# Kernel optimization log

Hardware: AMD Instinct MI355X
Metric: run time of the kernel (lower is better)

The kernel has to match this reference:

```python
import jax, jax.numpy as jnp
import numpy as np

C0 = 32   # number of 0e (scalar) channels
C1 = 16   # number of 1o (vector) channels
NG = 1024 # num_graphs
N = 300000
F = C0 * (C0 + 1) // 2 + C1 * (C1 + 1) // 2  # 664 invariant outputs of TensorSquare->0e


def setup_inputs() -> dict:
    key = jax.random.key(0)
    k1, k2, k3 = jax.random.split(key, 3)
    node_ft = jax.random.normal(k1, (N, C0 + 3 * C1), dtype=jnp.float32)
    batch_index = jnp.sort(jax.random.randint(k2, (N,), 0, NG, dtype=jnp.int32))
    # o3.Linear-style init: normal / sqrt(fan_in)
    W = jax.random.normal(k3, (F, 1), dtype=jnp.float32) / np.float32(np.sqrt(F))
    return {"node_ft": node_ft, "batch_index": batch_index, "num_graphs": NG, "W": W}


def tensor_square_0e(node_ft):
    # Equivariant tensor square keeping only 0e (invariant) outputs:
    #  - symmetric products of scalar channels s_i * s_j (i<=j)
    #  - dot products of vector channels v_i . v_j (i<=j), component-normalized
    s = node_ft[:, :C0]                      # [N, C0]
    v = node_ft[:, C0:].reshape(-1, C1, 3)   # [N, C1, 3]
    i0, j0 = jnp.triu_indices(C0)
    i1, j1 = jnp.triu_indices(C1)
    ts_s = s[:, i0] * s[:, j0]                                  # [N, 528]
    vdot = jnp.einsum('nic,njc->nij', v, v) / jnp.float32(np.sqrt(3.0))
    ts_v = vdot[:, i1, j1]                                      # [N, 136]
    return jnp.concatenate([ts_s, ts_v], axis=1)                # [N, 664]


def reference(node_ft, batch_index, num_graphs, W):
    x = tensor_square_0e(node_ft)            # [N, F]
    x = jax.nn.selu(x)
    x = x @ W                                # [N, 1] attention logits (1x0e)
    ex = jnp.exp(x)                          # [N, 1]
    z = jax.ops.segment_sum(ex, batch_index, num_segments=num_graphs)  # [G, 1]
    attn = ex / z[batch_index]               # segment softmax weights [N, 1]
    out = jax.ops.segment_sum(node_ft * attn, batch_index, num_segments=num_graphs)
    return out                               # [G, C0 + 3*C1]
```

## Files before the change

kernel.cpp:

```cpp
#include <hip/hip_runtime.h>


typedef float f2 __attribute__((ext_vector_type(2)));

#define C0 32
#define C1 16
#define NODE_F 80
#define NG_CONST 1024

#define SELU_SCALE 1.0507009873554804934193349852946
#define SELU_ALPHA 1.6732632423543772848170429916717
#define LOG2E      1.4426950408889634073599246810019

#define CS_SCALE 1.2011224087864498f
#define CV_SCALE 0.91271231102878545f

#define KS(i, j) ((i) * C0 - ((i) * ((i) -1)) / 2 + ((j) - (i)))
#define KV(i, j) (528 + (i) * C1 - ((i) * ((i) -1)) / 2 + ((j) - (i)))

__global__ __launch_bounds__(256, 4) void pass1_logits(
    const float* __restrict__ nf, const float* __restrict__ W,
    float* __restrict__ ex_out, int N)
{
    __shared__ float4 buf[128 * 20];
    const int tid = threadIdx.x;
    const int base_row = blockIdx.x * 256;
    const int total4 = N * 20;
    const float4* g4 = (const float4*)nf;

    float4 row4[20];
    const int half = tid >> 7;
    const int r    = tid & 127;

    #pragma unroll
    for (int it = 0; it < 10; ++it) {
        int g = base_row * 20 + it * 256 + tid;
        buf[it * 256 + tid] = g4[g < total4 ? g : 0];
    }
    __syncthreads();
    if (half == 0) {
        const float4* src = &buf[r * 20];
        #pragma unroll
        for (int q = 0; q < 20; ++q) row4[q] = src[q];
    }
    __syncthreads();
    #pragma unroll
    for (int it = 0; it < 10; ++it) {
        int g = (base_row + 128) * 20 + it * 256 + tid;
        buf[it * 256 + tid] = g4[g < total4 ? g : 0];
    }
    __syncthreads();
    if (half == 1) {
        const float4* src = &buf[r * 20];
        #pragma unroll
        for (int q = 0; q < 20; ++q) row4[q] = src[q];
    }

    const float* row = (const float*)row4;

    f2 accA[2], accB[2];
    accA[0] = 0.f; accA[1] = 0.f; accB[0] = 0.f; accB[1] = 0.f;

    {
        f2 s2[C0 / 2];
        #pragma unroll
        for (int q = 0; q < C0 / 2; ++q)
            s2[q] = f2{row[2 * q], row[2 * q + 1]} * CS_SCALE;

        #pragma unroll
        for (int i = 0; i < C0; ++i) {
            const float si = (i & 1) ? s2[i >> 1].y : s2[i >> 1].x;
            const f2 si2 = f2{si, si};
            #pragma unroll
            for (int q = i / 2; q < C0 / 2; ++q) {
                f2 f = si2 * s2[q];
                f2 p = __builtin_elementwise_max(f, (f2)0.f);
                f2 m = __builtin_elementwise_min(f, (f2)0.f);
                f2 e; e.x = __builtin_amdgcn_exp2f(m.x);
                      e.y = __builtin_amdgcn_exp2f(m.y);
                f2 w;
                w.x = (2 * q >= i) ? W[KS(i, 2 * q)] : 0.0f;
                w.y = W[KS(i, 2 * q + 1)];
                accA[q & 1] = __builtin_elementwise_fma(w, p, accA[q & 1]);
                accB[q & 1] = __builtin_elementwise_fma(w, e, accB[q & 1]);
            }
        }
    }

    {
        f2 vp[C1 / 2][3];
        #pragma unroll
        for (int q = 0; q < C1 / 2; ++q) {
            #pragma unroll
            for (int c = 0; c < 3; ++c)
                vp[q][c] = f2{row[C0 + 6 * q + c], row[C0 + 6 * q + 3 + c]} * CV_SCALE;
        }
        #pragma unroll
        for (int i = 0; i < C1; ++i) {
            const int iq = i >> 1;
            float vi0 = (i & 1) ? vp[iq][0].y : vp[iq][0].x;
            float vi1 = (i & 1) ? vp[iq][1].y : vp[iq][1].x;
            float vi2 = (i & 1) ? vp[iq][2].y : vp[iq][2].x;
            #pragma unroll
            for (int q = i / 2; q < C1 / 2; ++q) {
                f2 f = f2{vi0, vi0} * vp[q][0];
                f = __builtin_elementwise_fma(f2{vi1, vi1}, vp[q][1], f);
                f = __builtin_elementwise_fma(f2{vi2, vi2}, vp[q][2], f);
                f2 p = __builtin_elementwise_max(f, (f2)0.f);
                f2 m = __builtin_elementwise_min(f, (f2)0.f);
                f2 e; e.x = __builtin_amdgcn_exp2f(m.x);
                      e.y = __builtin_amdgcn_exp2f(m.y);
                f2 w;
                w.x = (2 * q >= i) ? W[KV(i, 2 * q)] : 0.0f;
                w.y = W[KV(i, 2 * q + 1)];
                accA[q & 1] = __builtin_elementwise_fma(w, p, accA[q & 1]);
                accB[q & 1] = __builtin_elementwise_fma(w, e, accB[q & 1]);
            }
        }
    }

    const float A1 = accA[0].x + accA[0].y + accA[1].x + accA[1].y;
    const float A2 = accB[0].x + accB[0].y + accB[1].x + accB[1].y;
    const float l2 = fmaf((float)SELU_SCALE, A1,
                          (float)(SELU_SCALE * SELU_ALPHA * LOG2E) * A2);
    const int n = base_row + tid;
    if (n < N) ex_out[n] = __builtin_amdgcn_exp2f(l2);
}

__global__ __launch_bounds__(256) void seg_bounds_kernel(
    const int* __restrict__ bi, int* __restrict__ bounds, int N)
{
    const int g = blockIdx.x * blockDim.x + threadIdx.x;
    if (g > NG_CONST) return;
    int lo = 0, hi = N;
    while (lo < hi) {
        int mid = (lo + hi) >> 1;
        if (bi[mid] < g) lo = mid + 1; else hi = mid;
    }
    bounds[g] = lo;
}

#define P2T 640

__global__ __launch_bounds__(P2T) void pass2_pool(
    const float* __restrict__ nf, const float* __restrict__ ex,
    const int* __restrict__ bounds, float* __restrict__ out)
{
    __shared__ float4 red4[P2T];
    __shared__ float  zred[P2T];
    const int g = blockIdx.x;
    const int tid = threadIdx.x;
    const int start = bounds[g];
    const int end   = bounds[g + 1];

    const int no = tid / 20;
    const int c4 = tid % 20;
    const float4* nf4 = (const float4*)nf;

    float4 a0 = make_float4(0.f, 0.f, 0.f, 0.f), a1 = a0;
    float  z0 = 0.f, z1 = 0.f;
    int n = start + no;
    for (; n + 32 < end; n += 64) {
        float  w0 = ex[n];
        float4 v0 = nf4[(size_t)n * 20 + c4];
        float  w1 = ex[n + 32];
        float4 v1 = nf4[(size_t)(n + 32) * 20 + c4];
        a0.x = fmaf(v0.x, w0, a0.x); a0.y = fmaf(v0.y, w0, a0.y);
        a0.z = fmaf(v0.z, w0, a0.z); a0.w = fmaf(v0.w, w0, a0.w);
        z0 += w0;
        a1.x = fmaf(v1.x, w1, a1.x); a1.y = fmaf(v1.y, w1, a1.y);
        a1.z = fmaf(v1.z, w1, a1.z); a1.w = fmaf(v1.w, w1, a1.w);
        z1 += w1;
    }
    if (n < end) {
        float  w0 = ex[n];
        float4 v0 = nf4[(size_t)n * 20 + c4];
        a0.x = fmaf(v0.x, w0, a0.x); a0.y = fmaf(v0.y, w0, a0.y);
        a0.z = fmaf(v0.z, w0, a0.z); a0.w = fmaf(v0.w, w0, a0.w);
        z0 += w0;
    }
    a0.x += a1.x; a0.y += a1.y; a0.z += a1.z; a0.w += a1.w;
    z0 += z1;

    red4[tid] = a0;
    zred[tid] = z0;
    __syncthreads();
    #pragma unroll
    for (int s = 16; s > 0; s >>= 1) {
        if (no < s) {
            float4 o = red4[tid + s * 20];
            red4[tid].x += o.x; red4[tid].y += o.y;
            red4[tid].z += o.z; red4[tid].w += o.w;
            zred[tid] += zred[tid + s * 20];
        }
        __syncthreads();
    }
    if (tid < 20) {
        float z = zred[tid];
        float inv_z = (z > 0.0f) ? (1.0f / z) : 0.0f;
        float4 r = red4[tid];
        r.x *= inv_z; r.y *= inv_z; r.z *= inv_z; r.w *= inv_z;
        ((float4*)(out + (size_t)g * NODE_F))[tid] = r;
    }
}

extern "C" void kernel_launch(void* const* d_in, const int* in_sizes, int n_in,
                              void* d_out, int out_size, void* d_ws, size_t ws_size,
                              hipStream_t stream) {
    const float* nf = (const float*)d_in[0];
    const int*   bi = (const int*)d_in[1];
    const float* W  = (const float*)d_in[3];
    float* out = (float*)d_out;

    const int N = in_sizes[0] / NODE_F;
    float* ex     = (float*)d_ws;
    int*   bounds = (int*)d_ws + N;

    hipLaunchKernelGGL(seg_bounds_kernel, dim3((NG_CONST + 256) / 256), dim3(256),
                       0, stream, bi, bounds, N);
    hipLaunchKernelGGL(pass1_logits, dim3((N + 255) / 256), dim3(256),
                       0, stream, nf, W, ex, N);
    hipLaunchKernelGGL(pass2_pool, dim3(NG_CONST), dim3(P2T),
                       0, stream, nf, ex, bounds, out);
}
```

Baseline: 201.9 us.

## Stage node features column-major in LDS and use rolled loops with padded W table

```diff
diff --git a/kernel.cpp b/kernel.cpp
--- a/kernel.cpp
+++ b/kernel.cpp
@@ -15,129 +15,132 @@
 #define CS_SCALE 1.2011224087864498f
 #define CV_SCALE 0.91271231102878545f
 
-#define KS(i, j) ((i) * C0 - ((i) * ((i) -1)) / 2 + ((j) - (i)))
-#define KV(i, j) (528 + (i) * C1 - ((i) * ((i) -1)) / 2 + ((j) - (i)))
-
-__global__ __launch_bounds__(256, 4) void pass1_logits(
-    const float* __restrict__ nf, const float* __restrict__ W,
+__device__ __forceinline__ int ks_idx(int i, int j) { return i * C0 - (i * (i - 1)) / 2 + (j - i); }
+__device__ __forceinline__ int kv_idx(int i, int j) { return 528 + i * C1 - (i * (i - 1)) / 2 + (j - i); }
+
+#define WS_OFF_WS 0
+#define WS_OFF_WV 1024
+#define WS_OFF_EX 1280
+
+__global__ __launch_bounds__(256) void prep_kernel(
+    const int* __restrict__ bi, const float* __restrict__ W,
+    float* __restrict__ ws, int* __restrict__ bounds, int N)
+{
+    const int t = blockIdx.x * blockDim.x + threadIdx.x;
+    if (t <= NG_CONST) {
+        int lo = 0, hi = N;
+        while (lo < hi) {
+            int mid = (lo + hi) >> 1;
+            if (bi[mid] < t) lo = mid + 1; else hi = mid;
+        }
+        bounds[t] = lo;
+    } else if (t < 1025 + 512) {
+        int u = t - 1025;
+        int i = u >> 4, q = u & 15;
+        int j0 = 2 * q, j1 = 2 * q + 1;
+        float x = (j0 >= i) ? W[ks_idx(i, j0)] : 0.0f;
+        float y = (j1 >= i) ? W[ks_idx(i, j1)] : 0.0f;
+        ws[WS_OFF_WS + 2 * u]     = x;
+        ws[WS_OFF_WS + 2 * u + 1] = y;
+    } else if (t < 1025 + 512 + 128) {
+        int u = t - 1537;
+        int i = u >> 3, q = u & 7;
+        int j0 = 2 * q, j1 = 2 * q + 1;
+        float x = (j0 >= i) ? W[kv_idx(i, j0)] : 0.0f;
+        float y = (j1 >= i) ? W[kv_idx(i, j1)] : 0.0f;
+        ws[WS_OFF_WV + 2 * u]     = x;
+        ws[WS_OFF_WV + 2 * u + 1] = y;
+    }
+}
+
+__global__ __launch_bounds__(256, 3) void pass1_logits(
+    const float* __restrict__ nf, const float* __restrict__ ws,
     float* __restrict__ ex_out, int N)
 {
-    __shared__ float4 buf[128 * 20];
-    const int tid = threadIdx.x;
-    const int base_row = blockIdx.x * 256;
-    const int total4 = N * 20;
+    __shared__ float lds[48 * 256];
+    const int tid  = threadIdx.x;
+    const int base = blockIdx.x * 256;
     const float4* g4 = (const float4*)nf;
-
-    float4 row4[20];
-    const int half = tid >> 7;
-    const int r    = tid & 127;
+    const f2* Ws = (const f2*)(ws + WS_OFF_WS);
+    const f2* Wv = (const f2*)(ws + WS_OFF_WV);
 
     #pragma unroll
-    for (int it = 0; it < 10; ++it) {
-        int g = base_row * 20 + it * 256 + tid;
-        buf[it * 256 + tid] = g4[g < total4 ? g : 0];
-    }
-    __syncthreads();
-    if (half == 0) {
-        const float4* src = &buf[r * 20];
-        #pragma unroll
-        for (int q = 0; q < 20; ++q) row4[q] = src[q];
-    }
-    __syncthreads();
+    for (int it = 0; it < 8; ++it) {
+        int idx = it * 256 + tid;
+        int r = idx >> 3, c4 = idx & 7;
+        int row = base + r; if (row > N - 1) row = N - 1;
+        float4 v = g4[(size_t)row * 20 + c4];
+        lds[(4 * c4 + 0) * 256 + r] = v.x * CS_SCALE;
+        lds[(4 * c4 + 1) * 256 + r] = v.y * CS_SCALE;
+        lds[(4 * c4 + 2) * 256 + r] = v.z * CS_SCALE;
+        lds[(4 * c4 + 3) * 256 + r] = v.w * CS_SCALE;
+    }
+    __syncthreads();
+
+    f2 accA = (f2)0.f, accB = (f2)0.f;
+
+    #pragma clang loop unroll(disable)
+    for (int i = 0; i < C0; ++i) {
+        const float si = lds[i * 256 + tid];
+        const f2* wrow = Ws + i * 16;
+        #pragma unroll 2
+        for (int q = i >> 1; q < 16; ++q) {
+            f2 sj = f2{lds[(2 * q) * 256 + tid], lds[(2 * q + 1) * 256 + tid]};
+            f2 f = sj * f2{si, si};
+            f2 p = __builtin_elementwise_max(f, (f2)0.f);
+            f2 m = __builtin_elementwise_min(f, (f2)0.f);
+            f2 e; e.x = __builtin_amdgcn_exp2f(m.x);
+                  e.y = __builtin_amdgcn_exp2f(m.y);
+            f2 w = wrow[q];
+            accA = __builtin_elementwise_fma(w, p, accA);
+            accB = __builtin_elementwise_fma(w, e, accB);
+        }
+    }
+    __syncthreads();
+
     #pragma unroll
-    for (int it = 0; it < 10; ++it) {
-        int g = (base_row + 128) * 20 + it * 256 + tid;
-        buf[it * 256 + tid] = g4[g < total4 ? g : 0];
-    }
-    __syncthreads();
-    if (half == 1) {
-        const float4* src = &buf[r * 20];
-        #pragma unroll
-        for (int q = 0; q < 20; ++q) row4[q] = src[q];
-    }
-
-    const float* row = (const float*)row4;
-
-    f2 accA[2], accB[2];
-    accA[0] = 0.f; accA[1] = 0.f; accB[0] = 0.f; accB[1] = 0.f;
-
-    {
-        f2 s2[C0 / 2];
-        #pragma unroll
-        for (int q = 0; q < C0 / 2; ++q)
-            s2[q] = f2{row[2 * q], row[2 * q + 1]} * CS_SCALE;
-
-        #pragma unroll
-        for (int i = 0; i < C0; ++i) {
-            const float si = (i & 1) ? s2[i >> 1].y : s2[i >> 1].x;
-            const f2 si2 = f2{si, si};
-            #pragma unroll
-            for (int q = i / 2; q < C0 / 2; ++q) {
-                f2 f = si2 * s2[q];
-                f2 p = __builtin_elementwise_max(f, (f2)0.f);
-                f2 m = __builtin_elementwise_min(f, (f2)0.f);
-                f2 e; e.x = __builtin_amdgcn_exp2f(m.x);
-                      e.y = __builtin_amdgcn_exp2f(m.y);
-                f2 w;
-                w.x = (2 * q >= i) ? W[KS(i, 2 * q)] : 0.0f;
-                w.y = W[KS(i, 2 * q + 1)];
-                accA[q & 1] = __builtin_elementwise_fma(w, p, accA[q & 1]);
-                accB[q & 1] = __builtin_elementwise_fma(w, e, accB[q & 1]);
-            }
-        }
-    }
-
-    {
-        f2 vp[C1 / 2][3];
-        #pragma unroll
-        for (int q = 0; q < C1 / 2; ++q) {
-            #pragma unroll
-            for (int c = 0; c < 3; ++c)
-                vp[q][c] = f2{row[C0 + 6 * q + c], row[C0 + 6 * q + 3 + c]} * CV_SCALE;
-        }
-        #pragma unroll
-        for (int i = 0; i < C1; ++i) {
-            const int iq = i >> 1;
-            float vi0 = (i & 1) ? vp[iq][0].y : vp[iq][0].x;
-            float vi1 = (i & 1) ? vp[iq][1].y : vp[iq][1].x;
-            float vi2 = (i & 1) ? vp[iq][2].y : vp[iq][2].x;
-            #pragma unroll
-            for (int q = i / 2; q < C1 / 2; ++q) {
-                f2 f = f2{vi0, vi0} * vp[q][0];
-                f = __builtin_elementwise_fma(f2{vi1, vi1}, vp[q][1], f);
-                f = __builtin_elementwise_fma(f2{vi2, vi2}, vp[q][2], f);
-                f2 p = __builtin_elementwise_max(f, (f2)0.f);
-                f2 m = __builtin_elementwise_min(f, (f2)0.f);
-                f2 e; e.x = __builtin_amdgcn_exp2f(m.x);
-                      e.y = __builtin_amdgcn_exp2f(m.y);
-                f2 w;
-                w.x = (2 * q >= i) ? W[KV(i, 2 * q)] : 0.0f;
-                w.y = W[KV(i, 2 * q + 1)];
-                accA[q & 1] = __builtin_elementwise_fma(w, p, accA[q & 1]);
-                accB[q & 1] = __builtin_elementwise_fma(w, e, accB[q & 1]);
-            }
-        }
-    }
-
-    const float A1 = accA[0].x + accA[0].y + accA[1].x + accA[1].y;
-    const float A2 = accB[0].x + accB[0].y + accB[1].x + accB[1].y;
+    for (int it = 0; it < 12; ++it) {
+        int idx = it * 256 + tid;
+        int r = idx / 12, c4 = idx % 12;
+        int row = base + r; if (row > N - 1) row = N - 1;
+        float4 v = g4[(size_t)row * 20 + 8 + c4];
+        lds[(4 * c4 + 0) * 256 + r] = v.x * CV_SCALE;
+        lds[(4 * c4 + 1) * 256 + r] = v.y * CV_SCALE;
+        lds[(4 * c4 + 2) * 256 + r] = v.z * CV_SCALE;
+        lds[(4 * c4 + 3) * 256 + r] = v.w * CV_SCALE;
+    }
+    __syncthreads();
+
+    #pragma clang loop unroll(disable)
+    for (int i = 0; i < C1; ++i) {
+        const float vi0 = lds[(3 * i + 0) * 256 + tid];
+        const float vi1 = lds[(3 * i + 1) * 256 + tid];
+        const float vi2 = lds[(3 * i + 2) * 256 + tid];
+        const f2* wrow = Wv + i * 8;
+        #pragma unroll 2
+        for (int q = i >> 1; q < 8; ++q) {
+            f2 vj0 = f2{lds[(6 * q + 0) * 256 + tid], lds[(6 * q + 3) * 256 + tid]};
+            f2 vj1 = f2{lds[(6 * q + 1) * 256 + tid], lds[(6 * q + 4) * 256 + tid]};
+            f2 vj2 = f2{lds[(6 * q + 2) * 256 + tid], lds[(6 * q + 5) * 256 + tid]};
+            f2 f = vj0 * f2{vi0, vi0};
+            f = __builtin_elementwise_fma(vj1, f2{vi1, vi1}, f);
+            f = __builtin_elementwise_fma(vj2, f2{vi2, vi2}, f);
+            f2 p = __builtin_elementwise_max(f, (f2)0.f);
+            f2 m = __builtin_elementwise_min(f, (f2)0.f);
+            f2 e; e.x = __builtin_amdgcn_exp2f(m.x);
+                  e.y = __builtin_amdgcn_exp2f(m.y);
+            f2 w = wrow[q];
+            accA = __builtin_elementwise_fma(w, p, accA);
+            accB = __builtin_elementwise_fma(w, e, accB);
+        }
+    }
+
+    const float A1 = accA.x + accA.y;
+    const float A2 = accB.x + accB.y;
     const float l2 = fmaf((float)SELU_SCALE, A1,
                           (float)(SELU_SCALE * SELU_ALPHA * LOG2E) * A2);
-    const int n = base_row + tid;
+    const int n = base + tid;
     if (n < N) ex_out[n] = __builtin_amdgcn_exp2f(l2);
-}
-
-__global__ __launch_bounds__(256) void seg_bounds_kernel(
-    const int* __restrict__ bi, int* __restrict__ bounds, int N)
-{
-    const int g = blockIdx.x * blockDim.x + threadIdx.x;
-    if (g > NG_CONST) return;
-    int lo = 0, hi = N;
-    while (lo < hi) {
-        int mid = (lo + hi) >> 1;
-        if (bi[mid] < g) lo = mid + 1; else hi = mid;
-    }
-    bounds[g] = lo;
 }
 
 #define P2T 640
@@ -213,13 +216,13 @@
     float* out = (float*)d_out;
 
     const int N = in_sizes[0] / NODE_F;
-    float* ex     = (float*)d_ws;
-    int*   bounds = (int*)d_ws + N;
-
-    hipLaunchKernelGGL(seg_bounds_kernel, dim3((NG_CONST + 256) / 256), dim3(256),
-                       0, stream, bi, bounds, N);
-    hipLaunchKernelGGL(pass1_logits, dim3((N + 255) / 256), dim3(256),
-                       0, stream, nf, W, ex, N);
-    hipLaunchKernelGGL(pass2_pool, dim3(NG_CONST), dim3(P2T),
-                       0, stream, nf, ex, bounds, out);
-}
+    float* ws     = (float*)d_ws;
+    float* ex     = ws + WS_OFF_EX;
+    int*   bounds = (int*)(ws + WS_OFF_EX + N);
+
+    hipLaunchKernelGGL(prep_kernel, dim3(7), dim3(256), 0, stream, bi, W, ws, bounds, N);
+    hipLaunchKernelGGL(pass1_logits, dim3((N + 255) / 256), dim3(256), 0, stream,
+                       nf, ws, ex, N);
+    hipLaunchKernelGGL(pass2_pool, dim3(NG_CONST), dim3(P2T), 0, stream,
+                       nf, ex, bounds, out);
+}
```

After: 221.0 us. 9.4% more time.

## Fuse logits and pooling into one kernel with atomic segment accumulation

Applied to the files above, without the earlier changes.

```diff
diff --git a/kernel.cpp b/kernel.cpp
--- a/kernel.cpp
+++ b/kernel.cpp
@@ -7,6 +7,7 @@
 #define C1 16
 #define NODE_F 80
 #define NG_CONST 1024
+#define NPB 320
 
 #define SELU_SCALE 1.0507009873554804934193349852946
 #define SELU_ALPHA 1.6732632423543772848170429916717
@@ -15,78 +16,91 @@
 #define CS_SCALE 1.2011224087864498f
 #define CV_SCALE 0.91271231102878545f
 
-#define KS(i, j) ((i) * C0 - ((i) * ((i) -1)) / 2 + ((j) - (i)))
-#define KV(i, j) (528 + (i) * C1 - ((i) * ((i) -1)) / 2 + ((j) - (i)))
-
-__global__ __launch_bounds__(256, 4) void pass1_logits(
-    const float* __restrict__ nf, const float* __restrict__ W,
-    float* __restrict__ ex_out, int N)
+#define WS_S 0
+#define WS_Z 81920
+#define WS_W 82944
+
+__device__ __forceinline__ int ks_idx(int i, int j) { return i * C0 - (i * (i - 1)) / 2 + (j - i); }
+__device__ __forceinline__ int kv_idx(int i, int j) { return 528 + i * C1 - (i * (i - 1)) / 2 + (j - i); }
+
+__global__ __launch_bounds__(256) void prep_kernel(
+    const float* __restrict__ W, float* __restrict__ ws)
 {
-    __shared__ float4 buf[128 * 20];
-    const int tid = threadIdx.x;
-    const int base_row = blockIdx.x * 256;
-    const int total4 = N * 20;
+    const int t = blockIdx.x * blockDim.x + threadIdx.x;
+    if (t < 82944) {
+        ws[t] = 0.0f;
+    } else {
+        int u = t - 82944;
+        if (u < 512) {
+            int i = u >> 4, q = u & 15;
+            int j0 = 2 * q, j1 = 2 * q + 1;
+            ws[WS_W + 2 * u]     = (j0 >= i) ? W[ks_idx(i, j0)] : 0.0f;
+            ws[WS_W + 2 * u + 1] = (j1 >= i) ? W[ks_idx(i, j1)] : 0.0f;
+        } else if (u < 640) {
+            int v = u - 512;
+            int i = v >> 3, q = v & 7;
+            int j0 = 2 * q, j1 = 2 * q + 1;
+            ws[WS_W + 1024 + 2 * v]     = (j0 >= i) ? W[kv_idx(i, j0)] : 0.0f;
+            ws[WS_W + 1024 + 2 * v + 1] = (j1 >= i) ? W[kv_idx(i, j1)] : 0.0f;
+        }
+    }
+}
+
+__global__ __launch_bounds__(NPB, 2) void main_kernel(
+    const float* __restrict__ nf, const int* __restrict__ bi,
+    const float* __restrict__ ws, float* __restrict__ S,
+    float* __restrict__ z, int N)
+{
+    __shared__ __align__(16) float Wlds[1280];
+    __shared__ float exl[NPB];
+    __shared__ int   bil[NPB];
+
+    const int tid  = threadIdx.x;
+    const int base = blockIdx.x * NPB;
     const float4* g4 = (const float4*)nf;
 
+    #pragma unroll
+    for (int u = tid; u < 1280; u += NPB) Wlds[u] = ws[WS_W + u];
+
+    const int  n     = base + tid;
+    const bool valid = (n < N);
+    const int  nn    = valid ? n : (N - 1);
+    bil[tid] = bi[nn];
+    __syncthreads();
+
     float4 row4[20];
-    const int half = tid >> 7;
-    const int r    = tid & 127;
-
     #pragma unroll
-    for (int it = 0; it < 10; ++it) {
-        int g = base_row * 20 + it * 256 + tid;
-        buf[it * 256 + tid] = g4[g < total4 ? g : 0];
-    }
-    __syncthreads();
-    if (half == 0) {
-        const float4* src = &buf[r * 20];
-        #pragma unroll
-        for (int q = 0; q < 20; ++q) row4[q] = src[q];
-    }
-    __syncthreads();
-    #pragma unroll
-    for (int it = 0; it < 10; ++it) {
-        int g = (base_row + 128) * 20 + it * 256 + tid;
-        buf[it * 256 + tid] = g4[g < total4 ? g : 0];
-    }
-    __syncthreads();
-    if (half == 1) {
-        const float4* src = &buf[r * 20];
-        #pragma unroll
-        for (int q = 0; q < 20; ++q) row4[q] = src[q];
-    }
-
+    for (int q = 0; q < 20; ++q) row4[q] = g4[(size_t)nn * 20 + q];
     const float* row = (const float*)row4;
 
+    const f2* WsL = (const f2*)Wlds;
+    const f2* WvL = (const f2*)(Wlds + 1024);
+
     f2 accA[2], accB[2];
-    accA[0] = 0.f; accA[1] = 0.f; accB[0] = 0.f; accB[1] = 0.f;
+    accA[0] = (f2)0.f; accA[1] = (f2)0.f; accB[0] = (f2)0.f; accB[1] = (f2)0.f;
 
     {
         f2 s2[C0 / 2];
         #pragma unroll
         for (int q = 0; q < C0 / 2; ++q)
             s2[q] = f2{row[2 * q], row[2 * q + 1]} * CS_SCALE;
-
         #pragma unroll
         for (int i = 0; i < C0; ++i) {
             const float si = (i & 1) ? s2[i >> 1].y : s2[i >> 1].x;
             const f2 si2 = f2{si, si};
             #pragma unroll
-            for (int q = i / 2; q < C0 / 2; ++q) {
+            for (int q = i >> 1; q < C0 / 2; ++q) {
                 f2 f = si2 * s2[q];
                 f2 p = __builtin_elementwise_max(f, (f2)0.f);
                 f2 m = __builtin_elementwise_min(f, (f2)0.f);
                 f2 e; e.x = __builtin_amdgcn_exp2f(m.x);
                       e.y = __builtin_amdgcn_exp2f(m.y);
-                f2 w;
-                w.x = (2 * q >= i) ? W[KS(i, 2 * q)] : 0.0f;
-                w.y = W[KS(i, 2 * q + 1)];
+                f2 w = WsL[i * 16 + q];
                 accA[q & 1] = __builtin_elementwise_fma(w, p, accA[q & 1]);
                 accB[q & 1] = __builtin_elementwise_fma(w, e, accB[q & 1]);
             }
         }
     }
-
     {
         f2 vp[C1 / 2][3];
         #pragma unroll
@@ -98,21 +112,19 @@
         #pragma unroll
         for (int i = 0; i < C1; ++i) {
             const int iq = i >> 1;
-            float vi0 = (i & 1) ? vp[iq][0].y : vp[iq][0].x;
-            float vi1 = (i & 1) ? vp[iq][1].y : vp[iq][1].x;
-            float vi2 = (i & 1) ? vp[iq][2].y : vp[iq][2].x;
+            const float vi0 = (i & 1) ? vp[iq][0].y : vp[iq][0].x;
+            const float vi1 = (i & 1) ? vp[iq][1].y : vp[iq][1].x;
+            const float vi2 = (i & 1) ? vp[iq][2].y : vp[iq][2].x;
             #pragma unroll
-            for (int q = i / 2; q < C1 / 2; ++q) {
-                f2 f = f2{vi0, vi0} * vp[q][0];
-                f = __builtin_elementwise_fma(f2{vi1, vi1}, vp[q][1], f);
-                f = __builtin_elementwise_fma(f2{vi2, vi2}, vp[q][2], f);
+            for (int q = i >> 1; q < C1 / 2; ++q) {
+                f2 f = vp[q][0] * f2{vi0, vi0};
+                f = __builtin_elementwise_fma(vp[q][1], f2{vi1, vi1}, f);
+                f = __builtin_elementwise_fma(vp[q][2], f2{vi2, vi2}, f);
                 f2 p = __builtin_elementwise_max(f, (f2)0.f);
                 f2 m = __builtin_elementwise_min(f, (f2)0.f);
                 f2 e; e.x = __builtin_amdgcn_exp2f(m.x);
                       e.y = __builtin_amdgcn_exp2f(m.y);
-                f2 w;
-                w.x = (2 * q >= i) ? W[KV(i, 2 * q)] : 0.0f;
-                w.y = W[KV(i, 2 * q + 1)];
+                f2 w = WvL[i * 8 + q];
                 accA[q & 1] = __builtin_elementwise_fma(w, p, accA[q & 1]);
                 accB[q & 1] = __builtin_elementwise_fma(w, e, accB[q & 1]);
             }
@@ -123,85 +135,49 @@
     const float A2 = accB[0].x + accB[0].y + accB[1].x + accB[1].y;
     const float l2 = fmaf((float)SELU_SCALE, A1,
                           (float)(SELU_SCALE * SELU_ALPHA * LOG2E) * A2);
-    const int n = base_row + tid;
-    if (n < N) ex_out[n] = __builtin_amdgcn_exp2f(l2);
-}
-
-__global__ __launch_bounds__(256) void seg_bounds_kernel(
-    const int* __restrict__ bi, int* __restrict__ bounds, int N)
-{
-    const int g = blockIdx.x * blockDim.x + threadIdx.x;
-    if (g > NG_CONST) return;
-    int lo = 0, hi = N;
-    while (lo < hi) {
-        int mid = (lo + hi) >> 1;
-        if (bi[mid] < g) lo = mid + 1; else hi = mid;
-    }
-    bounds[g] = lo;
-}
-
-#define P2T 640
-
-__global__ __launch_bounds__(P2T) void pass2_pool(
-    const float* __restrict__ nf, const float* __restrict__ ex,
-    const int* __restrict__ bounds, float* __restrict__ out)
-{
-    __shared__ float4 red4[P2T];
-    __shared__ float  zred[P2T];
-    const int g = blockIdx.x;
-    const int tid = threadIdx.x;
-    const int start = bounds[g];
-    const int end   = bounds[g + 1];
+    exl[tid] = valid ? __builtin_amdgcn_exp2f(l2) : 0.0f;
+    __syncthreads();
 
     const int no = tid / 20;
     const int c4 = tid % 20;
-    const float4* nf4 = (const float4*)nf;
-
-    float4 a0 = make_float4(0.f, 0.f, 0.f, 0.f), a1 = a0;
-    float  z0 = 0.f, z1 = 0.f;
-    int n = start + no;
-    for (; n + 32 < end; n += 64) {
-        float  w0 = ex[n];
-        float4 v0 = nf4[(size_t)n * 20 + c4];
-        float  w1 = ex[n + 32];
-        float4 v1 = nf4[(size_t)(n + 32) * 20 + c4];
-        a0.x = fmaf(v0.x, w0, a0.x); a0.y = fmaf(v0.y, w0, a0.y);
-        a0.z = fmaf(v0.z, w0, a0.z); a0.w = fmaf(v0.w, w0, a0.w);
-        z0 += w0;
-        a1.x = fmaf(v1.x, w1, a1.x); a1.y = fmaf(v1.y, w1, a1.y);
-        a1.z = fmaf(v1.z, w1, a1.z); a1.w = fmaf(v1.w, w1, a1.w);
-        z1 += w1;
-    }
-    if (n < end) {
-        float  w0 = ex[n];
-        float4 v0 = nf4[(size_t)n * 20 + c4];
-        a0.x = fmaf(v0.x, w0, a0.x); a0.y = fmaf(v0.y, w0, a0.y);
-        a0.z = fmaf(v0.z, w0, a0.z); a0.w = fmaf(v0.w, w0, a0.w);
-        z0 += w0;
-    }
-    a0.x += a1.x; a0.y += a1.y; a0.z += a1.z; a0.w += a1.w;
-    z0 += z1;
-
-    red4[tid] = a0;
-    zred[tid] = z0;
-    __syncthreads();
+    int cg = bil[no * 20];
+    float4 acc = make_float4(0.f, 0.f, 0.f, 0.f);
+    float  zacc = 0.0f;
+
     #pragma unroll
-    for (int s = 16; s > 0; s >>= 1) {
-        if (no < s) {
-            float4 o = red4[tid + s * 20];
-            red4[tid].x += o.x; red4[tid].y += o.y;
-            red4[tid].z += o.z; red4[tid].w += o.w;
-            zred[tid] += zred[tid + s * 20];
-        }
-        __syncthreads();
-    }
-    if (tid < 20) {
-        float z = zred[tid];
-        float inv_z = (z > 0.0f) ? (1.0f / z) : 0.0f;
-        float4 r = red4[tid];
-        r.x *= inv_z; r.y *= inv_z; r.z *= inv_z; r.w *= inv_z;
-        ((float4*)(out + (size_t)g * NODE_F))[tid] = r;
-    }
+    for (int k = 0; k < 20; ++k) {
+        const int nl = no * 20 + k;
+        const int g2 = bil[nl];
+        if (g2 != cg) {
+            unsafeAtomicAdd(&S[cg * NODE_F + c4 * 4 + 0], acc.x);
+            unsafeAtomicAdd(&S[cg * NODE_F + c4 * 4 + 1], acc.y);
+            unsafeAtomicAdd(&S[cg * NODE_F + c4 * 4 + 2], acc.z);
+            unsafeAtomicAdd(&S[cg * NODE_F + c4 * 4 + 3], acc.w);
+            if (c4 == 0) unsafeAtomicAdd(&z[cg], zacc);
+            acc = make_float4(0.f, 0.f, 0.f, 0.f); zacc = 0.0f; cg = g2;
+        }
+        int idx = base + nl; if (idx > N - 1) idx = N - 1;
+        const float  w = exl[nl];
+        const float4 v = g4[(size_t)idx * 20 + c4];
+        acc.x = fmaf(v.x, w, acc.x); acc.y = fmaf(v.y, w, acc.y);
+        acc.z = fmaf(v.z, w, acc.z); acc.w = fmaf(v.w, w, acc.w);
+        zacc += w;
+    }
+    unsafeAtomicAdd(&S[cg * NODE_F + c4 * 4 + 0], acc.x);
+    unsafeAtomicAdd(&S[cg * NODE_F + c4 * 4 + 1], acc.y);
+    unsafeAtomicAdd(&S[cg * NODE_F + c4 * 4 + 2], acc.z);
+    unsafeAtomicAdd(&S[cg * NODE_F + c4 * 4 + 3], acc.w);
+    if (c4 == 0) unsafeAtomicAdd(&z[cg], zacc);
+}
+
+__global__ __launch_bounds__(256) void divide_kernel(
+    const float* __restrict__ S, const float* __restrict__ z,
+    float* __restrict__ out)
+{
+    const int t = blockIdx.x * blockDim.x + threadIdx.x;
+    if (t >= NG_CONST * NODE_F) return;
+    const float zz = z[t / NODE_F];
+    out[t] = (zz > 0.0f) ? (S[t] / zz) : 0.0f;
 }
 
 extern "C" void kernel_launch(void* const* d_in, const int* in_sizes, int n_in,
@@ -213,13 +189,13 @@
     float* out = (float*)d_out;
 
     const int N = in_sizes[0] / NODE_F;
-    float* ex     = (float*)d_ws;
-    int*   bounds = (int*)d_ws + N;
-
-    hipLaunchKernelGGL(seg_bounds_kernel, dim3((NG_CONST + 256) / 256), dim3(256),
-                       0, stream, bi, bounds, N);
-    hipLaunchKernelGGL(pass1_logits, dim3((N + 255) / 256), dim3(256),
-                       0, stream, nf, W, ex, N);
-    hipLaunchKernelGGL(pass2_pool, dim3(NG_CONST), dim3(P2T),
-                       0, stream, nf, ex, bounds, out);
-}
+    float* ws = (float*)d_ws;
+    float* S  = ws + WS_S;
+    float* z  = ws + WS_Z;
+
+    hipLaunchKernelGGL(prep_kernel, dim3(332), dim3(256), 0, stream, W, ws);
+    hipLaunchKernelGGL(main_kernel, dim3((N + NPB - 1) / NPB), dim3(NPB), 0, stream,
+                       nf, bi, ws, S, z, N);
+    hipLaunchKernelGGL(divide_kernel, dim3((NG_CONST * NODE_F + 255) / 256), dim3(256),
+                       0, stream, S, z, out);
+}
```

Result: faster. 195.2 us (-3.3%).
